# Kernel tuning notes

Measured on AMD Instinct MI355X. Metric: run time of the kernel, lower is better.

## Reference

```python
import jax, jax.numpy as jnp
import numpy as np

EPS = 1e-8  # torch nn.CosineSimilarity default eps


def setup_inputs() -> dict:
    key = jax.random.key(0)
    k1, k2, k3 = jax.random.split(key, 3)
    N, K, Q, CH, H, W, D = 32, 5, 15, 3, 84, 84, 1600
    supp_x = jax.random.normal(k1, (N, K, CH, H, W), dtype=jnp.float32)
    query_x = jax.random.normal(k2, (N, Q, CH, H, W), dtype=jnp.float32)
    W_enc = jax.random.normal(k3, (CH * H * W, D), dtype=jnp.float32) * 0.02
    return {"supp_x": supp_x, "query_x": query_x, "W_enc": W_enc}


def reference(supp_x, query_x, W_enc):
    N, K = supp_x.shape[0], supp_x.shape[1]
    Q = query_x.shape[1]
    # encoder: flatten image -> linear projection (stands in for backbone)
    s_feat = supp_x.reshape(N * K, -1) @ W_enc          # (N*K, D)
    x_proto = s_feat.reshape(N, K, -1).mean(axis=1)     # (N, D) class prototypes
    x_q = query_x.reshape(N * Q, -1) @ W_enc            # (N*Q, D)
    # cosine similarity: L2-normalize with eps clamp, then single matmul
    qn = x_q / jnp.maximum(jnp.linalg.norm(x_q, axis=1, keepdims=True), EPS)
    pn = x_proto / jnp.maximum(jnp.linalg.norm(x_proto, axis=1, keepdims=True), EPS)
    sim = qn @ pn.T                                     # (N*Q, N)
    return jax.nn.log_softmax(sim, axis=1)
```

## Files before the change

kernel.cpp:

```cpp
#include <hip/hip_runtime.h>
#include <cstdint>
#include <cstddef>

namespace {

constexpr int NCLS   = 32;
constexpr int KSHOT  = 5;
constexpr int FDIM   = 21168;
constexpr int KPAD   = 21248;
constexpr int DDIM   = 1600;
constexpr int NROW   = 512;
constexpr int NQROW  = 480;
constexpr int NKT    = 332;
constexpr int MAXS   = 10;

using short8 = __attribute__((ext_vector_type(8))) short;
using f32x4  = __attribute__((ext_vector_type(4))) float;

__device__ __forceinline__ unsigned f2bf(float x) {
    union { float f; unsigned u; } v; v.f = x;
    unsigned r = v.u + 0x7fffu + ((v.u >> 16) & 1u);
    return r >> 16;
}

__global__ void prep_A(const float* __restrict__ supp,
                       const float* __restrict__ query,
                       unsigned short* __restrict__ A) {
    const int r = blockIdx.y;
    const int u = blockIdx.x * blockDim.x + threadIdx.x;
    if (u >= KPAD / 4) return;
    const int c = u * 4;
    float4 v = make_float4(0.f, 0.f, 0.f, 0.f);
    if (c < FDIM) {
        if (r < NCLS) {
            const float* s = supp + (size_t)r * KSHOT * FDIM + c;
            float4 a0 = *(const float4*)(s);
            float4 a1 = *(const float4*)(s + FDIM);
            float4 a2 = *(const float4*)(s + 2 * FDIM);
            float4 a3 = *(const float4*)(s + 3 * FDIM);
            float4 a4 = *(const float4*)(s + 4 * FDIM);
            v.x = (a0.x + a1.x + a2.x + a3.x + a4.x) * 0.2f;
            v.y = (a0.y + a1.y + a2.y + a3.y + a4.y) * 0.2f;
            v.z = (a0.z + a1.z + a2.z + a3.z + a4.z) * 0.2f;
            v.w = (a0.w + a1.w + a2.w + a3.w + a4.w) * 0.2f;
        } else {
            v = *(const float4*)(query + (size_t)(r - NCLS) * FDIM + c);
        }
    }
    ushort4 o;
    o.x = (unsigned short)f2bf(v.x); o.y = (unsigned short)f2bf(v.y);
    o.z = (unsigned short)f2bf(v.z); o.w = (unsigned short)f2bf(v.w);
    *(ushort4*)(A + (size_t)r * KPAD + c) = o;
}

__global__ __launch_bounds__(512, 4) void gemm11(
        const unsigned short* __restrict__ A,
        const float* __restrict__ W,
        float* __restrict__ Cpart, int S) {
    __shared__ unsigned short Al[2][256 * 64];
    __shared__ unsigned short Bl[2][64 * 64];

    const int nwg = gridDim.x, orig = blockIdx.x;
    const int xcd = orig & 7, q8 = nwg >> 3, r8 = nwg & 7;
    const int wgid = (xcd < r8 ? xcd * (q8 + 1) : r8 * (q8 + 1) + (xcd - r8) * q8)
                   + (orig >> 3);

    const int s   = wgid / 50;
    const int rem = wgid % 50;
    const int mt  = rem & 1;
    const int nt  = rem >> 1;
    const int m0  = mt * 256;
    const int n0  = nt * 64;
    const int t0  = (NKT * s) / S;
    const int t1  = (NKT * (s + 1)) / S;
    const int tmax = t1 - 1;

    const int tid  = threadIdx.x;
    const int lane = tid & 63;
    const int w    = tid >> 6;
    const int wr   = w & 3;
    const int wc   = w >> 2;
    const int g    = lane >> 4;
    const int r15  = lane & 15;

    const int srow = lane >> 3, sblk = lane & 7;
    const unsigned short* Asrc[4];
    int AdstOff[4];
    #pragma unroll
    for (int i = 0; i < 4; ++i) {
        const int r = w * 32 + i * 8 + srow;
        Asrc[i] = A + (size_t)(m0 + r) * KPAD + (size_t)((sblk ^ (r & 7)) * 8);
        AdstOff[i] = (w * 32 + i * 8) * 64;
    }

    const int np = tid & 31;
    const int kq = tid >> 5;
    const float* Wp = W + n0 + 2 * np;
    const int bws = (kq ^ (2 * (np & 7)) ^ (8 * ((np >> 3) & 1))) * 4;
    const int wb0 = (2 * np) * 64 + bws;
    const int wb1 = (2 * np + 1) * 64 + bws;

    f32x4 acc[4][2];
    #pragma unroll
    for (int i = 0; i < 4; ++i)
        #pragma unroll
        for (int j = 0; j < 2; ++j)
            acc[i][j] = (f32x4){0.f, 0.f, 0.f, 0.f};

    float2 wv[4];

#define LOAD_W(t) { const int kb_ = (t) * 64 + kq * 4; _Pragma("unroll") \
    for (int i = 0; i < 4; ++i) \
        wv[i] = (kb_ + i < FDIM) ? *(const float2*)(Wp + (size_t)(kb_ + i) * DDIM) \
                                 : make_float2(0.f, 0.f); }

#define PACK_B(buf) { uint2 p0_, p1_; \
    p0_.x = f2bf(wv[0].x) | (f2bf(wv[1].x) << 16); \
    p0_.y = f2bf(wv[2].x) | (f2bf(wv[3].x) << 16); \
    p1_.x = f2bf(wv[0].y) | (f2bf(wv[1].y) << 16); \
    p1_.y = f2bf(wv[2].y) | (f2bf(wv[3].y) << 16); \
    *(uint2*)&Bl[buf][wb0] = p0_; *(uint2*)&Bl[buf][wb1] = p1_; }

#define GLDS_A(buf, t) { _Pragma("unroll") \
    for (int i = 0; i < 4; ++i) \
        __builtin_amdgcn_global_load_lds( \
            (const __attribute__((address_space(1))) void*)(Asrc[i] + (size_t)(t) * 64), \
            (__attribute__((address_space(3))) void*)(&Al[buf][AdstOff[i]]), 16, 0, 0); }

#define COMPUTE(buf) { _Pragma("unroll") \
    for (int kk = 0; kk < 2; ++kk) { \
        const int q_ = kk * 4 + g; \
        short8 bf_[2], af_[4]; \
        _Pragma("unroll") \
        for (int ns = 0; ns < 2; ++ns) { \
            const int n_ = wc * 32 + ns * 16 + r15; \
            const int rb_ = q_ ^ ((n_ >> 1) & 7) ^ (4 * ((n_ >> 4) & 1)); \
            bf_[ns] = *(const short8*)&Bl[buf][n_ * 64 + rb_ * 8]; \
        } \
        _Pragma("unroll") \
        for (int ms = 0; ms < 4; ++ms) { \
            const int R_ = wr * 64 + ms * 16 + r15; \
            af_[ms] = *(const short8*)&Al[buf][R_ * 64 + ((q_ ^ (R_ & 7)) * 8)]; \
        } \
        _Pragma("unroll") \
        for (int ms = 0; ms < 4; ++ms) \
            _Pragma("unroll") \
            for (int ns = 0; ns < 2; ++ns) \
                acc[ms][ns] = __builtin_amdgcn_mfma_f32_16x16x32_bf16( \
                    af_[ms], bf_[ns], acc[ms][ns], 0, 0, 0); } }

    LOAD_W(t0);
    PACK_B(0);
    LOAD_W(min(t0 + 1, tmax));
    GLDS_A(0, t0);
    __syncthreads();

    int cur = 0;
    for (int t = t0; t < t1; ++t) {
        const bool m1 = (t + 1 < t1);
        if (m1) {
            PACK_B(cur ^ 1);
            LOAD_W(min(t + 2, tmax));
            GLDS_A(cur ^ 1, t + 1);
        }
        COMPUTE(cur);
        __syncthreads();
        if (m1) cur ^= 1;
    }

#undef LOAD_W
#undef PACK_B
#undef GLDS_A
#undef COMPUTE

    float* Cp = Cpart + (size_t)s * NROW * DDIM;
    #pragma unroll
    for (int ms = 0; ms < 4; ++ms) {
        const int row = m0 + wr * 64 + ms * 16 + g * 4;
        #pragma unroll
        for (int ns = 0; ns < 2; ++ns) {
            const int col = n0 + wc * 32 + ns * 16 + r15;
            #pragma unroll
            for (int r = 0; r < 4; ++r)
                Cp[(size_t)(row + r) * DDIM + col] = acc[ms][ns][r];
        }
    }
}

__global__ void reduce_norm(const float* __restrict__ Cpart,
                            float* __restrict__ C,
                            float* __restrict__ inv_norm, int S) {
    const int row = blockIdx.x;
    const int tid = threadIdx.x;
    float acc = 0.f;
    for (int c4 = tid * 4; c4 < DDIM; c4 += 1024) {
        float4 v = make_float4(0.f, 0.f, 0.f, 0.f);
        for (int s2 = 0; s2 < S; ++s2) {
            float4 p = *(const float4*)&Cpart[((size_t)s2 * NROW + row) * DDIM + c4];
            v.x += p.x; v.y += p.y; v.z += p.z; v.w += p.w;
        }
        *(float4*)&C[(size_t)row * DDIM + c4] = v;
        acc += v.x * v.x + v.y * v.y + v.z * v.z + v.w * v.w;
    }
    __shared__ float red[4];
    #pragma unroll
    for (int off = 32; off > 0; off >>= 1) acc += __shfl_xor(acc, off);
    if ((tid & 63) == 0) red[tid >> 6] = acc;
    __syncthreads();
    if (tid == 0) {
        float a = red[0] + red[1] + red[2] + red[3];
        inv_norm[row] = 1.f / fmaxf(sqrtf(a), 1e-8f);
    }
}

__global__ void simlog(const float* __restrict__ C,
                       const float* __restrict__ inv_norm,
                       float* __restrict__ out) {
    __shared__ float qs[DDIM];
    __shared__ float sims[NCLS];
    const int r = blockIdx.x;
    const int tid = threadIdx.x;
    const float* qrow = C + (size_t)(NCLS + r) * DDIM;
    for (int c = tid; c < DDIM; c += 256) qs[c] = qrow[c];
    __syncthreads();
    const float invq = inv_norm[NCLS + r];
    const int lane = tid & 63, w = tid >> 6;
    #pragma unroll
    for (int j = 0; j < 8; ++j) {
        const int p = w * 8 + j;
        const float* prow = C + (size_t)p * DDIM;
        float d = 0.f;
        for (int c = lane; c < DDIM; c += 64) d += qs[c] * prow[c];
        #pragma unroll
        for (int off = 32; off > 0; off >>= 1) d += __shfl_xor(d, off);
        if (lane == 0) sims[p] = d * invq * inv_norm[p];
    }
    __syncthreads();
    if (w == 0) {
        float v = (lane < NCLS) ? sims[lane] : -1e30f;
        float m = v;
        #pragma unroll
        for (int off = 32; off > 0; off >>= 1) m = fmaxf(m, __shfl_xor(m, off));
        float e = (lane < NCLS) ? expf(v - m) : 0.f;
        float ss = e;
        #pragma unroll
        for (int off = 32; off > 0; off >>= 1) ss += __shfl_xor(ss, off);
        if (lane < NCLS) out[(size_t)r * NCLS + lane] = v - m - logf(ss);
    }
}

}


extern "C" void kernel_launch(void* const* d_in, const int* in_sizes, int n_in,
                              void* d_out, int out_size, void* d_ws, size_t ws_size,
                              hipStream_t stream) {
    const float* supp  = (const float*)d_in[0];
    const float* query = (const float*)d_in[1];
    const float* Wenc  = (const float*)d_in[2];
    float* out = (float*)d_out;

    const size_t fixedA = 21757952;
    const size_t slot   = (size_t)NROW * DDIM * 4;

    int S = MAXS;
    if (ws_size > fixedA + slot + 4096) {
        size_t avail = (ws_size - fixedA - slot - 4096) / slot;
        if ((size_t)S > avail) S = (int)avail;
    }
    if (S < 1) S = 1;

    char* ws = (char*)d_ws;
    unsigned short* A = (unsigned short*)ws;
    float* Cpart    = (float*)(ws + fixedA);
    float* C        = (float*)(ws + fixedA + (size_t)S * slot);
    float* inv_norm = (float*)(ws + fixedA + (size_t)(S + 1) * slot);

    hipLaunchKernelGGL(prep_A, dim3((KPAD / 4 + 255) / 256, NROW), dim3(256),
                       0, stream, supp, query, A);
    hipLaunchKernelGGL(gemm11, dim3(50 * S), dim3(512), 0, stream,
                       A, Wenc, Cpart, S);
    hipLaunchKernelGGL(reduce_norm, dim3(NROW), dim3(256), 0, stream,
                       Cpart, C, inv_norm, S);
    hipLaunchKernelGGL(simlog, dim3(NQROW), dim3(256), 0, stream,
                       C, inv_norm, out);
}
```

Baseline: 132.2 us.

## Enlarge GEMM tile to 256x256 and raise split-K count

The GEMM workgroup tile grows from 256x64 to 256x256, so each wave computes 128x64 outputs with 8x4 MFMA accumulators. W is loaded as float4 over 8 k-rows and packed into a new swizzled LDS layout. The split-K maximum rises to 18 so the smaller number of tiles (14 per split) still fills the GPU. The aim is more reuse of A and B per LDS load and fewer redundant global reads of W. The cost is more registers and LDS (occupancy bound lowered to 2), padding waste in the last N tile since 1600 is not a multiple of 256, and more partial sums for the reduction kernel to combine.

```diff
diff --git a/kernel.cpp b/kernel.cpp
--- a/kernel.cpp
+++ b/kernel.cpp
@@ -1,4 +1,5 @@
 #include <hip/hip_runtime.h>
+#include <hip/hip_bf16.h>
 #include <cstdint>
 #include <cstddef>
 
@@ -12,15 +13,22 @@
 constexpr int NROW   = 512;
 constexpr int NQROW  = 480;
 constexpr int NKT    = 332;
-constexpr int MAXS   = 10;
+constexpr int MAXS   = 18;
 
 using short8 = __attribute__((ext_vector_type(8))) short;
 using f32x4  = __attribute__((ext_vector_type(4))) float;
 
-__device__ __forceinline__ unsigned f2bf(float x) {
+__device__ __forceinline__ unsigned short f2bf(float x) {
     union { float f; unsigned u; } v; v.f = x;
     unsigned r = v.u + 0x7fffu + ((v.u >> 16) & 1u);
-    return r >> 16;
+    return (unsigned short)(r >> 16);
+}
+
+__device__ __forceinline__ unsigned short f2bfc(float x) {
+    __hip_bfloat16 h = __float2bfloat16(x);
+    unsigned short u;
+    __builtin_memcpy(&u, &h, 2);
+    return u;
 }
 
 __global__ void prep_A(const float* __restrict__ supp,
@@ -48,29 +56,28 @@
         }
     }
     ushort4 o;
-    o.x = (unsigned short)f2bf(v.x); o.y = (unsigned short)f2bf(v.y);
-    o.z = (unsigned short)f2bf(v.z); o.w = (unsigned short)f2bf(v.w);
+    o.x = f2bf(v.x); o.y = f2bf(v.y); o.z = f2bf(v.z); o.w = f2bf(v.w);
     *(ushort4*)(A + (size_t)r * KPAD + c) = o;
 }
 
-__global__ __launch_bounds__(512, 4) void gemm11(
+__global__ __launch_bounds__(512, 2) void gemm13(
         const unsigned short* __restrict__ A,
         const float* __restrict__ W,
         float* __restrict__ Cpart, int S) {
     __shared__ unsigned short Al[2][256 * 64];
-    __shared__ unsigned short Bl[2][64 * 64];
+    __shared__ unsigned short Bl[2][256 * 64];
 
     const int nwg = gridDim.x, orig = blockIdx.x;
     const int xcd = orig & 7, q8 = nwg >> 3, r8 = nwg & 7;
     const int wgid = (xcd < r8 ? xcd * (q8 + 1) : r8 * (q8 + 1) + (xcd - r8) * q8)
                    + (orig >> 3);
 
-    const int s   = wgid / 50;
-    const int rem = wgid % 50;
+    const int s   = wgid / 14;
+    const int rem = wgid % 14;
     const int mt  = rem & 1;
     const int nt  = rem >> 1;
     const int m0  = mt * 256;
-    const int n0  = nt * 64;
+    const int n0  = nt * 256;
     const int t0  = (NKT * s) / S;
     const int t1  = (NKT * (s + 1)) / S;
     const int tmax = t1 - 1;
@@ -78,8 +85,8 @@
     const int tid  = threadIdx.x;
     const int lane = tid & 63;
     const int w    = tid >> 6;
-    const int wr   = w & 3;
-    const int wc   = w >> 2;
+    const int wr   = w & 1;
+    const int wc   = w >> 1;
     const int g    = lane >> 4;
     const int r15  = lane & 15;
 
@@ -93,33 +100,52 @@
         AdstOff[i] = (w * 32 + i * 8) * 64;
     }
 
-    const int np = tid & 31;
-    const int kq = tid >> 5;
-    const float* Wp = W + n0 + 2 * np;
-    const int bws = (kq ^ (2 * (np & 7)) ^ (8 * ((np >> 3) & 1))) * 4;
-    const int wb0 = (2 * np) * 64 + bws;
-    const int wb1 = (2 * np + 1) * 64 + bws;
-
-    f32x4 acc[4][2];
-    #pragma unroll
-    for (int i = 0; i < 4; ++i)
-        #pragma unroll
-        for (int j = 0; j < 2; ++j)
+    const int nq = tid & 63;
+    const int kh = tid >> 6;
+    const int ncb = min(n0 + 4 * nq, DDIM - 4);
+    const float* Wp = W + ncb;
+    const int bq = (kh ^ (nq & 7)) * 8;
+
+    f32x4 acc[8][4];
+    #pragma unroll
+    for (int i = 0; i < 8; ++i)
+        #pragma unroll
+        for (int j = 0; j < 4; ++j)
             acc[i][j] = (f32x4){0.f, 0.f, 0.f, 0.f};
 
-    float2 wv[4];
-
-#define LOAD_W(t) { const int kb_ = (t) * 64 + kq * 4; _Pragma("unroll") \
-    for (int i = 0; i < 4; ++i) \
-        wv[i] = (kb_ + i < FDIM) ? *(const float2*)(Wp + (size_t)(kb_ + i) * DDIM) \
-                                 : make_float2(0.f, 0.f); }
-
-#define PACK_B(buf) { uint2 p0_, p1_; \
-    p0_.x = f2bf(wv[0].x) | (f2bf(wv[1].x) << 16); \
-    p0_.y = f2bf(wv[2].x) | (f2bf(wv[3].x) << 16); \
-    p1_.x = f2bf(wv[0].y) | (f2bf(wv[1].y) << 16); \
-    p1_.y = f2bf(wv[2].y) | (f2bf(wv[3].y) << 16); \
-    *(uint2*)&Bl[buf][wb0] = p0_; *(uint2*)&Bl[buf][wb1] = p1_; }
+    float4 wv[8];
+
+#define LOAD_W(t) { const int kb_ = (t) * 64 + kh * 8; _Pragma("unroll") \
+    for (int i = 0; i < 8; ++i) { \
+        const int k_ = kb_ + i; \
+        wv[i] = (k_ < FDIM) ? *(const float4*)(Wp + (size_t)k_ * DDIM) \
+                            : make_float4(0.f, 0.f, 0.f, 0.f); } }
+
+#define PACK_B(buf) { \
+    { uint4 P; \
+      P.x = f2bfc(wv[0].x) | ((unsigned)f2bfc(wv[1].x) << 16); \
+      P.y = f2bfc(wv[2].x) | ((unsigned)f2bfc(wv[3].x) << 16); \
+      P.z = f2bfc(wv[4].x) | ((unsigned)f2bfc(wv[5].x) << 16); \
+      P.w = f2bfc(wv[6].x) | ((unsigned)f2bfc(wv[7].x) << 16); \
+      *(uint4*)&Bl[buf][(4 * nq + 0) * 64 + bq] = P; } \
+    { uint4 P; \
+      P.x = f2bfc(wv[0].y) | ((unsigned)f2bfc(wv[1].y) << 16); \
+      P.y = f2bfc(wv[2].y) | ((unsigned)f2bfc(wv[3].y) << 16); \
+      P.z = f2bfc(wv[4].y) | ((unsigned)f2bfc(wv[5].y) << 16); \
+      P.w = f2bfc(wv[6].y) | ((unsigned)f2bfc(wv[7].y) << 16); \
+      *(uint4*)&Bl[buf][(4 * nq + 1) * 64 + bq] = P; } \
+    { uint4 P; \
+      P.x = f2bfc(wv[0].z) | ((unsigned)f2bfc(wv[1].z) << 16); \
+      P.y = f2bfc(wv[2].z) | ((unsigned)f2bfc(wv[3].z) << 16); \
+      P.z = f2bfc(wv[4].z) | ((unsigned)f2bfc(wv[5].z) << 16); \
+      P.w = f2bfc(wv[6].z) | ((unsigned)f2bfc(wv[7].z) << 16); \
+      *(uint4*)&Bl[buf][(4 * nq + 2) * 64 + bq] = P; } \
+    { uint4 P; \
+      P.x = f2bfc(wv[0].w) | ((unsigned)f2bfc(wv[1].w) << 16); \
+      P.y = f2bfc(wv[2].w) | ((unsigned)f2bfc(wv[3].w) << 16); \
+      P.z = f2bfc(wv[4].w) | ((unsigned)f2bfc(wv[5].w) << 16); \
+      P.w = f2bfc(wv[6].w) | ((unsigned)f2bfc(wv[7].w) << 16); \
+      *(uint4*)&Bl[buf][(4 * nq + 3) * 64 + bq] = P; } }
 
 #define GLDS_A(buf, t) { _Pragma("unroll") \
     for (int i = 0; i < 4; ++i) \
@@ -130,29 +156,25 @@
 #define COMPUTE(buf) { _Pragma("unroll") \
     for (int kk = 0; kk < 2; ++kk) { \
         const int q_ = kk * 4 + g; \
-        short8 bf_[2], af_[4]; \
+        short8 bf_[4]; \
         _Pragma("unroll") \
-        for (int ns = 0; ns < 2; ++ns) { \
-            const int n_ = wc * 32 + ns * 16 + r15; \
-            const int rb_ = q_ ^ ((n_ >> 1) & 7) ^ (4 * ((n_ >> 4) & 1)); \
-            bf_[ns] = *(const short8*)&Bl[buf][n_ * 64 + rb_ * 8]; \
+        for (int ns = 0; ns < 4; ++ns) { \
+            const int n_ = wc * 64 + ns * 16 + r15; \
+            bf_[ns] = *(const short8*)&Bl[buf][n_ * 64 + ((q_ ^ ((n_ >> 2) & 7)) * 8)]; \
         } \
         _Pragma("unroll") \
-        for (int ms = 0; ms < 4; ++ms) { \
-            const int R_ = wr * 64 + ms * 16 + r15; \
-            af_[ms] = *(const short8*)&Al[buf][R_ * 64 + ((q_ ^ (R_ & 7)) * 8)]; \
-        } \
-        _Pragma("unroll") \
-        for (int ms = 0; ms < 4; ++ms) \
+        for (int ms = 0; ms < 8; ++ms) { \
+            const int R_ = wr * 128 + ms * 16 + r15; \
+            short8 af_ = *(const short8*)&Al[buf][R_ * 64 + ((q_ ^ (R_ & 7)) * 8)]; \
             _Pragma("unroll") \
-            for (int ns = 0; ns < 2; ++ns) \
+            for (int ns = 0; ns < 4; ++ns) \
                 acc[ms][ns] = __builtin_amdgcn_mfma_f32_16x16x32_bf16( \
-                    af_[ms], bf_[ns], acc[ms][ns], 0, 0, 0); } }
+                    af_, bf_[ns], acc[ms][ns], 0, 0, 0); } } }
 
     LOAD_W(t0);
     PACK_B(0);
+    GLDS_A(0, t0);
     LOAD_W(min(t0 + 1, tmax));
-    GLDS_A(0, t0);
     __syncthreads();
 
     int cur = 0;
@@ -175,14 +197,16 @@
 
     float* Cp = Cpart + (size_t)s * NROW * DDIM;
     #pragma unroll
-    for (int ms = 0; ms < 4; ++ms) {
-        const int row = m0 + wr * 64 + ms * 16 + g * 4;
-        #pragma unroll
-        for (int ns = 0; ns < 2; ++ns) {
-            const int col = n0 + wc * 32 + ns * 16 + r15;
-            #pragma unroll
-            for (int r = 0; r < 4; ++r)
-                Cp[(size_t)(row + r) * DDIM + col] = acc[ms][ns][r];
+    for (int ms = 0; ms < 8; ++ms) {
+        const int row = m0 + wr * 128 + ms * 16 + g * 4;
+        #pragma unroll
+        for (int ns = 0; ns < 4; ++ns) {
+            const int col = n0 + wc * 64 + ns * 16 + r15;
+            if (col < DDIM) {
+                #pragma unroll
+                for (int r = 0; r < 4; ++r)
+                    Cp[(size_t)(row + r) * DDIM + col] = acc[ms][ns][r];
+            }
         }
     }
 }
@@ -278,7 +302,7 @@
 
     hipLaunchKernelGGL(prep_A, dim3((KPAD / 4 + 255) / 256, NROW), dim3(256),
                        0, stream, supp, query, A);
-    hipLaunchKernelGGL(gemm11, dim3(50 * S), dim3(512), 0, stream,
+    hipLaunchKernelGGL(gemm13, dim3(14 * S), dim3(512), 0, stream,
                        A, Wenc, Cpart, S);
     hipLaunchKernelGGL(reduce_norm, dim3(NROW), dim3(256), 0, stream,
                        Cpart, C, inv_norm, S);
```

Result: slower. 157.2 us (+18.9%).
